# Kernel optimization log

Hardware: AMD Instinct MI355X
Metric: run time of the kernel (lower is better)

## Reference

```python
import jax, jax.numpy as jnp
import numpy as np

ALPHA = 0.2  # LeakyReLU negative slope


def setup_inputs() -> dict:
    key = jax.random.key(0)
    k1, k2, k3, k4 = jax.random.split(key, 4)
    B, N, F_IN, F_OUT = 4, 4096, 256, 256
    h = jax.random.normal(k1, (B, N, F_IN), dtype=jnp.float32)
    adj = jax.random.randint(k2, (B, N, N), 0, 2, dtype=jnp.int32)
    # xavier_normal with gain=1.414: std = gain*sqrt(2/(fan_in+fan_out))
    std_W = 1.414 * np.sqrt(2.0 / (F_IN + F_OUT))
    W = jax.random.normal(k3, (F_IN, F_OUT), dtype=jnp.float32) * std_W
    std_a = 1.414 * np.sqrt(2.0 / (1 + 2 * F_OUT))
    a = jax.random.normal(k4, (1, 2 * F_OUT), dtype=jnp.float32) * std_a
    return {"h": h, "adj": adj, "W": W, "a": a}


def reference(h, adj, W, a):
    # h: [B, N, F_in], adj: [B, N, N] (0/1), W: [F_in, F_out], a: [1, 2*F_out]
    F_out = W.shape[1]
    Hh = jnp.einsum('bni,io->bno', h, W)               # [B, N, F_out]
    a_src = a[0, :F_out]                                # attends to edge source i
    a_dst = a[0, F_out:]                                # attends to edge target j
    s = jnp.einsum('bno,o->bn', Hh, a_src)              # [B, N]
    d = jnp.einsum('bno,o->bn', Hh, a_dst)              # [B, N]
    # score(i,j) = a . concat(Hh_i, Hh_j) = s_i + d_j
    logits = s[:, :, None] + d[:, None, :]              # [B, N, N]
    # edge_e = exp(-leakyrelu(score)) only on edges (adj nonzero), else 0
    e = jnp.where(adj != 0,
                  jnp.exp(-jax.nn.leaky_relu(logits, negative_slope=ALPHA)),
                  jnp.zeros((), dtype=Hh.dtype))        # [B, N, N]
    rowsum = jnp.sum(e, axis=-1, keepdims=True)         # [B, N, 1]
    # rows with zero sum keep divisor 1 (as in the torch code)
    rowsum = jnp.where(rowsum == 0.0, 1.0, rowsum)
    h_prime = jnp.einsum('bnm,bmo->bno', e, Hh) / rowsum  # [B, N, F_out]
    return jax.nn.elu(h_prime)  # concat=True branch
```

## Files before the change

kernel.cpp:

```cpp
#include <hip/hip_runtime.h>

#define LRELU_ALPHA 0.2f

typedef __bf16 bf16x8 __attribute__((ext_vector_type(8)));
typedef unsigned short u16;
typedef unsigned short u16x8 __attribute__((ext_vector_type(8)));
typedef float f32x4 __attribute__((ext_vector_type(4)));
typedef int int4v __attribute__((ext_vector_type(4)));

__device__ __forceinline__ u16 f2bf(float f) {
  unsigned int u = __float_as_uint(f);
  u += 0x7fffu + ((u >> 16) & 1u);
  return (u16)(u >> 16);
}

__device__ __forceinline__ void gload16(const void* g, void* lds) {
  __builtin_amdgcn_global_load_lds(
      (const __attribute__((address_space(1))) void*)g,
      (__attribute__((address_space(3))) void*)lds, 16, 0, 0);
}

__global__ __launch_bounds__(256) void wcast(const float* __restrict__ W,
                                             u16* __restrict__ WbT) {
  int idx = blockIdx.x * 256 + threadIdx.x;
  WbT[idx] = f2bf(W[(idx & 255) * 256 + (idx >> 8)]);
}

__global__ __launch_bounds__(256) void gemm1(const float* __restrict__ h,
                                             const u16* __restrict__ WbT,
                                             const float* __restrict__ a,
                                             u16* __restrict__ HhT,
                                             float* __restrict__ sbuf,
                                             float* __restrict__ dbuf) {
  const int tid = threadIdx.x, bid = blockIdx.x;
  const int l = tid & 63, w = tid >> 6;
  const int lr = l & 15;
  const int lk = (l >> 4) << 3;
  const int rowA = bid * 64 + 16 * w + lr;
  const float* hrow = h + (size_t)rowA * 256 + lk;

  f32x4 acc[16];
#pragma unroll
  for (int n = 0; n < 16; ++n) acc[n] = (f32x4){0.f, 0.f, 0.f, 0.f};

  for (int k0 = 0; k0 < 256; k0 += 32) {
    f32x4 a0 = *(const f32x4*)(hrow + k0);
    f32x4 a1 = *(const f32x4*)(hrow + k0 + 4);
    u16x8 au;
    au[0] = f2bf(a0[0]); au[1] = f2bf(a0[1]); au[2] = f2bf(a0[2]); au[3] = f2bf(a0[3]);
    au[4] = f2bf(a1[0]); au[5] = f2bf(a1[1]); au[6] = f2bf(a1[2]); au[7] = f2bf(a1[3]);
    bf16x8 af = __builtin_bit_cast(bf16x8, au);
#pragma unroll
    for (int n = 0; n < 16; ++n) {
      int4v bv = *(const int4v*)(WbT + (size_t)(16 * n + lr) * 256 + k0 + lk);
      bf16x8 bf = __builtin_bit_cast(bf16x8, bv);
      acc[n] = __builtin_amdgcn_mfma_f32_16x16x32_bf16(af, bf, acc[n], 0, 0, 0);
    }
  }

  float sp[4] = {0.f, 0.f, 0.f, 0.f}, dp[4] = {0.f, 0.f, 0.f, 0.f};
#pragma unroll
  for (int n = 0; n < 16; ++n) {
    int col = 16 * n + lr;
    float as = a[col];
    float ad = a[256 + col];
#pragma unroll
    for (int rr = 0; rr < 4; ++rr) {
      int row = bid * 64 + 16 * w + ((l >> 4) << 2) + rr;
      int bb = row >> 12, nl = row & 4095;
      float v = acc[n][rr];
      HhT[((size_t)(bb * 256 + col)) * 4096 + nl] = f2bf(v);
      sp[rr] += v * as;
      dp[rr] += v * ad;
    }
  }
#pragma unroll
  for (int rr = 0; rr < 4; ++rr) {
#pragma unroll
    for (int off = 1; off < 16; off <<= 1) {
      sp[rr] += __shfl_xor(sp[rr], off);
      dp[rr] += __shfl_xor(dp[rr], off);
    }
  }
  if ((l & 15) == 0) {
#pragma unroll
    for (int rr = 0; rr < 4; ++rr) {
      int row = bid * 64 + 16 * w + ((l >> 4) << 2) + rr;
      sbuf[row] = sp[rr];
      dbuf[row] = dp[rr];
    }
  }
}

__global__ __launch_bounds__(256, 2) void gat_main(const int* __restrict__ adj,
                                                   const u16* __restrict__ HhT,
                                                   const float* __restrict__ s,
                                                   const float* __restrict__ d,
                                                   float* __restrict__ out) {
  __shared__ __align__(16) u16 Bt[3][8192];
  __shared__ __align__(16) int At[3][1024];
  __shared__ __align__(16) float Dt[3][32];
  __shared__ float rs_lds[32];

  const int tid = threadIdx.x, bid = blockIdx.x;
  const int xcd = bid & 7;
  const int b = xcd >> 1;
  const int tile = (bid >> 3) | ((xcd & 1) << 6);
  const int rowbase = tile << 5;

  const int l = tid & 63, w = tid >> 6;
  const int lr = l & 15, lkg = l >> 4;
  const int row0 = 16 * (w & 1);
  const int colb = 128 * (w >> 1);

  const int myrow = rowbase + row0 + lr;
  const float s_row = s[b * 4096 + myrow];

  const char* HhTb = (const char*)HhT + (size_t)b * 2097152;
  const int colg0 = (w * 4) * 16 + (l >> 2);
  const int csB = (l & 3) ^ ((l >> 3) & 3);
  const char* bsrcBase = HhTb + (size_t)colg0 * 8192 + csB * 16;
  const int csA = (l & 7) ^ (l >> 3);
  const char* asrc = (const char*)adj +
      ((size_t)(b * 4096 + rowbase + w * 8 + (l >> 3))) * 16384 + csA * 16;
  const char* dsrc = (const char*)d + (size_t)b * 16384 + (l & 7) * 16;

  char* BtB = (char*)&Bt[0][0];
  char* AtB = (char*)&At[0][0];
  char* DtB = (char*)&Dt[0][0];

  const int atoff0 = (row0 + lr) * 128 + (((2 * lkg) ^ (lr & 7)) * 16);
  const int atoff1 = (row0 + lr) * 128 + (((2 * lkg + 1) ^ (lr & 7)) * 16);
  const int btbase = (colb + lr) * 64 + ((lkg ^ ((lr >> 1) & 3)) * 16);
  const int dtoff = lkg * 32;

  f32x4 acc[8];
#pragma unroll
  for (int n = 0; n < 8; ++n) acc[n] = (f32x4){0.f, 0.f, 0.f, 0.f};
  float racc = 0.f;

#define ISSUE(NXT, STEP)                                                      \
  {                                                                           \
    const size_t bo_ = (size_t)(STEP) * 64;                                   \
    const size_t ao_ = (size_t)(STEP) * 128;                                  \
    gload16(bsrcBase + bo_,          BtB + (NXT) * 16384 + (w * 4 + 0) * 1024); \
    gload16(bsrcBase + bo_ + 131072, BtB + (NXT) * 16384 + (w * 4 + 1) * 1024); \
    gload16(bsrcBase + bo_ + 262144, BtB + (NXT) * 16384 + (w * 4 + 2) * 1024); \
    gload16(bsrcBase + bo_ + 393216, BtB + (NXT) * 16384 + (w * 4 + 3) * 1024); \
    gload16(asrc + ao_,              AtB + (NXT) * 4096 + w * 1024);          \
    if (l < 8) gload16(dsrc + ao_,   DtB + (NXT) * 128);                      \
  }

#define COMPUTE(CUR)                                                          \
  {                                                                           \
    int4v aA = *(const int4v*)(AtB + (CUR) * 4096 + atoff0);                  \
    int4v aB = *(const int4v*)(AtB + (CUR) * 4096 + atoff1);                  \
    f32x4 dA = *(const f32x4*)(DtB + (CUR) * 128 + dtoff);                    \
    f32x4 dB = *(const f32x4*)(DtB + (CUR) * 128 + dtoff + 16);               \
    u16x8 au_;                                                                \
    {                                                                         \
      int aj[8] = {aA.x, aA.y, aA.z, aA.w, aB.x, aB.y, aB.z, aB.w};           \
      float dv[8] = {dA[0], dA[1], dA[2], dA[3], dB[0], dB[1], dB[2], dB[3]}; \
      _Pragma("unroll")                                                       \
      for (int j = 0; j < 8; ++j) {                                           \
        float lg = s_row + dv[j];                                             \
        float t = fmaxf(lg, LRELU_ALPHA * lg);                                \
        float e = (aj[j] != 0) ? __expf(-t) : 0.f;                            \
        racc += e;                                                            \
        au_[j] = f2bf(e);                                                     \
      }                                                                       \
    }                                                                         \
    bf16x8 af = __builtin_bit_cast(bf16x8, au_);                              \
    _Pragma("unroll")                                                         \
    for (int n = 0; n < 8; ++n) {                                             \
      bf16x8 bfv = __builtin_bit_cast(bf16x8,                                 \
          *(const int4v*)(BtB + (CUR) * 16384 + btbase + n * 1024));          \
      acc[n] = __builtin_amdgcn_mfma_f32_16x16x32_bf16(af, bfv, acc[n],       \
                                                       0, 0, 0);              \
    }                                                                         \
  }

  ISSUE(0, 0)
  ISSUE(1, 1)
  asm volatile("s_waitcnt vmcnt(6)" ::: "memory");
  __builtin_amdgcn_s_barrier();

  for (int k = 0; k < 126; k += 3) {
    ISSUE(2, k + 2)
    COMPUTE(0)
    asm volatile("s_waitcnt lgkmcnt(0)" ::: "memory");
    asm volatile("s_waitcnt vmcnt(6)" ::: "memory");
    __builtin_amdgcn_s_barrier();

    ISSUE(0, k + 3)
    COMPUTE(1)
    asm volatile("s_waitcnt lgkmcnt(0)" ::: "memory");
    asm volatile("s_waitcnt vmcnt(6)" ::: "memory");
    __builtin_amdgcn_s_barrier();

    ISSUE(1, k + 4)
    COMPUTE(2)
    asm volatile("s_waitcnt lgkmcnt(0)" ::: "memory");
    asm volatile("s_waitcnt vmcnt(6)" ::: "memory");
    __builtin_amdgcn_s_barrier();
  }
  COMPUTE(0)
  asm volatile("s_waitcnt lgkmcnt(0)" ::: "memory");
  asm volatile("s_waitcnt vmcnt(0)" ::: "memory");
  __builtin_amdgcn_s_barrier();
  COMPUTE(1)
#undef ISSUE
#undef COMPUTE

  racc += __shfl_xor(racc, 16);
  racc += __shfl_xor(racc, 32);
  if (w < 2 && lkg == 0) rs_lds[row0 + lr] = (racc == 0.f) ? 1.f : racc;
  __syncthreads();

#pragma unroll
  for (int rr = 0; rr < 4; ++rr) {
    int rin = row0 + (lkg << 2) + rr;
    float inv = 1.f / rs_lds[rin];
    size_t obase = ((size_t)(b * 4096 + rowbase + rin)) * 256 + colb;
#pragma unroll
    for (int n = 0; n < 8; ++n) {
      float v = acc[n][rr] * inv;
      out[obase + 16 * n + lr] = v > 0.f ? v : (__expf(v) - 1.f);
    }
  }
}

extern "C" void kernel_launch(void* const* d_in, const int* in_sizes, int n_in,
                              void* d_out, int out_size, void* d_ws, size_t ws_size,
                              hipStream_t stream) {
  const float* h = (const float*)d_in[0];
  const int* adj = (const int*)d_in[1];
  const float* W = (const float*)d_in[2];
  const float* a = (const float*)d_in[3];
  float* out = (float*)d_out;

  u16* WbT  = (u16*)d_ws;
  u16* HhT  = (u16*)((char*)d_ws + 131072);
  float* sb = (float*)((char*)d_ws + 131072 + 8388608);
  float* db = sb + 16384;

  hipLaunchKernelGGL(wcast,    dim3(256), dim3(256), 0, stream, W, WbT);
  hipLaunchKernelGGL(gemm1,    dim3(256), dim3(256), 0, stream, h, WbT, a, HhT, sb, db);
  hipLaunchKernelGGL(gat_main, dim3(512), dim3(256), 0, stream, adj, HhT, sb, db, out);
}
```

Measured before the change: 196.9 us.

## Use 64-row tiles with 512-thread blocks, 4-stage pipeline, and MFMA priority

```diff
diff --git a/kernel.cpp b/kernel.cpp
--- a/kernel.cpp
+++ b/kernel.cpp
@@ -92,46 +92,44 @@
   }
 }
 
-__global__ __launch_bounds__(256, 2) void gat_main(const int* __restrict__ adj,
+__global__ __launch_bounds__(512, 2) void gat_main(const int* __restrict__ adj,
                                                    const u16* __restrict__ HhT,
                                                    const float* __restrict__ s,
                                                    const float* __restrict__ d,
                                                    float* __restrict__ out) {
-  __shared__ __align__(16) u16 Bt[3][8192];
-  __shared__ __align__(16) int At[3][1024];
-  __shared__ __align__(16) float Dt[3][32];
-  __shared__ float rs_lds[32];
+  __shared__ __align__(16) u16 Bt4[4][8192];
+  __shared__ __align__(16) int At4[4][2048];
+  __shared__ __align__(16) float Dt4[4][32];
+  __shared__ float rs_lds[64];
 
   const int tid = threadIdx.x, bid = blockIdx.x;
   const int xcd = bid & 7;
-  const int b = xcd >> 1;
-  const int tile = (bid >> 3) | ((xcd & 1) << 6);
-  const int rowbase = tile << 5;
+  const int t256 = (xcd << 5) | (bid >> 3);
+  const int b = t256 >> 6;
+  const int rowbase = (t256 & 63) << 6;
 
   const int l = tid & 63, w = tid >> 6;
+  const int wr = w & 3, wc = w >> 2;
   const int lr = l & 15, lkg = l >> 4;
-  const int row0 = 16 * (w & 1);
-  const int colb = 128 * (w >> 1);
-
-  const int myrow = rowbase + row0 + lr;
-  const float s_row = s[b * 4096 + myrow];
+  const int rowt = 16 * wr + lr;
+  const float s_row = s[b * 4096 + rowbase + rowt];
 
   const char* HhTb = (const char*)HhT + (size_t)b * 2097152;
-  const int colg0 = (w * 4) * 16 + (l >> 2);
   const int csB = (l & 3) ^ ((l >> 3) & 3);
-  const char* bsrcBase = HhTb + (size_t)colg0 * 8192 + csB * 16;
+  const char* bsrc0 = HhTb + (size_t)(w * 32 +      (l >> 2)) * 8192 + csB * 16;
+  const char* bsrc1 = HhTb + (size_t)(w * 32 + 16 + (l >> 2)) * 8192 + csB * 16;
   const int csA = (l & 7) ^ (l >> 3);
   const char* asrc = (const char*)adj +
       ((size_t)(b * 4096 + rowbase + w * 8 + (l >> 3))) * 16384 + csA * 16;
-  const char* dsrc = (const char*)d + (size_t)b * 16384 + (l & 7) * 16;
-
-  char* BtB = (char*)&Bt[0][0];
-  char* AtB = (char*)&At[0][0];
-  char* DtB = (char*)&Dt[0][0];
-
-  const int atoff0 = (row0 + lr) * 128 + (((2 * lkg) ^ (lr & 7)) * 16);
-  const int atoff1 = (row0 + lr) * 128 + (((2 * lkg + 1) ^ (lr & 7)) * 16);
-  const int btbase = (colb + lr) * 64 + ((lkg ^ ((lr >> 1) & 3)) * 16);
+  const char* dsrc = (const char*)d + (size_t)b * 16384 + w * 16;
+
+  char* BtB = (char*)&Bt4[0][0];
+  char* AtB = (char*)&At4[0][0];
+  char* DtB = (char*)&Dt4[0][0];
+
+  const int atoff0 = rowt * 128 + (((2 * lkg)     ^ (lr & 7)) * 16);
+  const int atoff1 = rowt * 128 + (((2 * lkg + 1) ^ (lr & 7)) * 16);
+  const int btbase = (128 * wc + lr) * 64 + ((lkg ^ ((lr >> 1) & 3)) * 16);
   const int dtoff = lkg * 32;
 
   f32x4 acc[8];
@@ -141,20 +139,17 @@
 
 #define ISSUE(NXT, STEP)                                                      \
   {                                                                           \
-    const size_t bo_ = (size_t)(STEP) * 64;                                   \
-    const size_t ao_ = (size_t)(STEP) * 128;                                  \
-    gload16(bsrcBase + bo_,          BtB + (NXT) * 16384 + (w * 4 + 0) * 1024); \
-    gload16(bsrcBase + bo_ + 131072, BtB + (NXT) * 16384 + (w * 4 + 1) * 1024); \
-    gload16(bsrcBase + bo_ + 262144, BtB + (NXT) * 16384 + (w * 4 + 2) * 1024); \
-    gload16(bsrcBase + bo_ + 393216, BtB + (NXT) * 16384 + (w * 4 + 3) * 1024); \
-    gload16(asrc + ao_,              AtB + (NXT) * 4096 + w * 1024);          \
-    if (l < 8) gload16(dsrc + ao_,   DtB + (NXT) * 128);                      \
+    const size_t st_ = (size_t)(STEP);                                        \
+    gload16(bsrc0 + st_ * 64,  BtB + (NXT) * 16384 + (w * 2 + 0) * 1024);     \
+    gload16(bsrc1 + st_ * 64,  BtB + (NXT) * 16384 + (w * 2 + 1) * 1024);     \
+    gload16(asrc + st_ * 128,  AtB + (NXT) * 8192 + w * 1024);                \
+    if (l == 0) gload16(dsrc + st_ * 128, DtB + (NXT) * 128 + w * 16);        \
   }
 
 #define COMPUTE(CUR)                                                          \
   {                                                                           \
-    int4v aA = *(const int4v*)(AtB + (CUR) * 4096 + atoff0);                  \
-    int4v aB = *(const int4v*)(AtB + (CUR) * 4096 + atoff1);                  \
+    int4v aA = *(const int4v*)(AtB + (CUR) * 8192 + atoff0);                  \
+    int4v aB = *(const int4v*)(AtB + (CUR) * 8192 + atoff1);                  \
     f32x4 dA = *(const f32x4*)(DtB + (CUR) * 128 + dtoff);                    \
     f32x4 dB = *(const f32x4*)(DtB + (CUR) * 128 + dtoff + 16);               \
     u16x8 au_;                                                                \
@@ -171,6 +166,7 @@
       }                                                                       \
     }                                                                         \
     bf16x8 af = __builtin_bit_cast(bf16x8, au_);                              \
+    __builtin_amdgcn_s_setprio(1);                                            \
     _Pragma("unroll")                                                         \
     for (int n = 0; n < 8; ++n) {                                             \
       bf16x8 bfv = __builtin_bit_cast(bf16x8,                                 \
@@ -178,50 +174,44 @@
       acc[n] = __builtin_amdgcn_mfma_f32_16x16x32_bf16(af, bfv, acc[n],       \
                                                        0, 0, 0);              \
     }                                                                         \
-  }
+    __builtin_amdgcn_s_setprio(0);                                            \
+  }
+
+#define WAITS(VN)                                                             \
+    asm volatile("s_waitcnt lgkmcnt(0)" ::: "memory");                        \
+    asm volatile("s_waitcnt vmcnt(" #VN ")" ::: "memory");                    \
+    __builtin_amdgcn_s_barrier();
 
   ISSUE(0, 0)
   ISSUE(1, 1)
-  asm volatile("s_waitcnt vmcnt(6)" ::: "memory");
+  ISSUE(2, 2)
+  asm volatile("s_waitcnt vmcnt(8)" ::: "memory");
   __builtin_amdgcn_s_barrier();
 
-  for (int k = 0; k < 126; k += 3) {
-    ISSUE(2, k + 2)
-    COMPUTE(0)
-    asm volatile("s_waitcnt lgkmcnt(0)" ::: "memory");
-    asm volatile("s_waitcnt vmcnt(6)" ::: "memory");
-    __builtin_amdgcn_s_barrier();
-
-    ISSUE(0, k + 3)
-    COMPUTE(1)
-    asm volatile("s_waitcnt lgkmcnt(0)" ::: "memory");
-    asm volatile("s_waitcnt vmcnt(6)" ::: "memory");
-    __builtin_amdgcn_s_barrier();
-
-    ISSUE(1, k + 4)
-    COMPUTE(2)
-    asm volatile("s_waitcnt lgkmcnt(0)" ::: "memory");
-    asm volatile("s_waitcnt vmcnt(6)" ::: "memory");
-    __builtin_amdgcn_s_barrier();
-  }
-  COMPUTE(0)
-  asm volatile("s_waitcnt lgkmcnt(0)" ::: "memory");
-  asm volatile("s_waitcnt vmcnt(0)" ::: "memory");
-  __builtin_amdgcn_s_barrier();
-  COMPUTE(1)
+  for (int k = 0; k < 124; k += 4) {
+    ISSUE(3, k + 3) COMPUTE(0) WAITS(8)
+    ISSUE(0, k + 4) COMPUTE(1) WAITS(8)
+    ISSUE(1, k + 5) COMPUTE(2) WAITS(8)
+    ISSUE(2, k + 6) COMPUTE(3) WAITS(8)
+  }
+  ISSUE(3, 127) COMPUTE(0) WAITS(8)
+  COMPUTE(1) WAITS(4)
+  COMPUTE(2) WAITS(0)
+  COMPUTE(3)
 #undef ISSUE
 #undef COMPUTE
+#undef WAITS
 
   racc += __shfl_xor(racc, 16);
   racc += __shfl_xor(racc, 32);
-  if (w < 2 && lkg == 0) rs_lds[row0 + lr] = (racc == 0.f) ? 1.f : racc;
+  if (wc == 0 && l < 16) rs_lds[16 * wr + l] = (racc == 0.f) ? 1.f : racc;
   __syncthreads();
 
 #pragma unroll
   for (int rr = 0; rr < 4; ++rr) {
-    int rin = row0 + (lkg << 2) + rr;
+    int rin = 16 * wr + (lkg << 2) + rr;
     float inv = 1.f / rs_lds[rin];
-    size_t obase = ((size_t)(b * 4096 + rowbase + rin)) * 256 + colb;
+    size_t obase = ((size_t)(b * 4096 + rowbase + rin)) * 256 + 128 * wc;
 #pragma unroll
     for (int n = 0; n < 8; ++n) {
       float v = acc[n][rr] * inv;
@@ -246,5 +236,5 @@
 
   hipLaunchKernelGGL(wcast,    dim3(256), dim3(256), 0, stream, W, WbT);
   hipLaunchKernelGGL(gemm1,    dim3(256), dim3(256), 0, stream, h, WbT, a, HhT, sb, db);
-  hipLaunchKernelGGL(gat_main, dim3(512), dim3(256), 0, stream, adj, HhT, sb, db, out);
-}
+  hipLaunchKernelGGL(gat_main, dim3(256), dim3(512), 0, stream, adj, HhT, sb, db, out);
+}
```

After: 176.2 us. 10.5% less time.
